# Optimization experiments

Hardware: AMD Instinct MI355X
Metric: run time of the kernel (lower is better)

The kernel has to match this reference:

```python
import jax, jax.numpy as jnp
import numpy as np

D_ATOM, D_PAIR, D_HID = 128, 64, 32
NF, NLOC = 1, 384


def setup_inputs() -> dict:
    key = jax.random.key(0)
    k1, k2, k3, k4, k5 = jax.random.split(key, 5)
    m = jax.random.normal(k1, (NF, NLOC, D_ATOM), dtype=jnp.float32)
    nlist = jax.random.randint(k2, (NF, NLOC, 32), 0, NLOC)
    op_mask = jnp.ones((1,), dtype=jnp.float32)
    op_norm = jnp.ones((1,), dtype=jnp.float32)
    # linear_in: d_atom -> 2*d_hid ; linear_out: d_hid**2 -> d_pair
    W_in = jax.random.normal(k3, (2 * D_HID, D_ATOM), dtype=jnp.float32) * 0.05
    b_in = jnp.zeros((2 * D_HID,), dtype=jnp.float32)
    W_out = jax.random.normal(k4, (D_PAIR, D_HID * D_HID), dtype=jnp.float32) * 0.05
    b_out = jnp.zeros((D_PAIR,), dtype=jnp.float32)
    return {"m": m, "nlist": nlist, "op_mask": op_mask, "op_norm": op_norm,
            "W_in": W_in, "b_in": b_in, "W_out": W_out, "b_out": b_out}


def reference(m, nlist, op_mask, op_norm, W_in, b_in, W_out, b_out):
    # ab: [nf, nloc, 2*d_hid]
    ab = jnp.einsum('fnd,hd->fnh', m, W_in) + b_in
    ab = ab * op_mask
    a, b = jnp.split(ab, 2, axis=-1)  # each [nf, nloc, d_hid]
    nf, nloc, d = a.shape
    # outer product: [nf, nloc, nloc, d_hid*d_hid]
    outer = jnp.einsum('fix,fjy->fijxy', a, b).reshape(nf, nloc, nloc, d * d)
    z = jnp.einsum('fijk,pk->fijp', outer, W_out) + b_out  # [nf, nloc, nloc, d_pair]
    return z * op_norm
```

## Files before the change

kernel.cpp:

```cpp
#include <hip/hip_runtime.h>

#define NLOC 384


__global__ __launch_bounds__(256) void k_ab(const float* __restrict__ m,
                                            const float* __restrict__ W_in,
                                            const float* __restrict__ b_in,
                                            const float* __restrict__ op_mask,
                                            float* __restrict__ ab) {
    const int t  = threadIdx.x;
    const int h  = t & 63;
    const int ng = __builtin_amdgcn_readfirstlane(t >> 6);
    const int n  = blockIdx.x * 4 + ng;
    const float* mrow = m + n * 128;
    const float* wrow = W_in + h * 128;
    float acc = 0.f;
#pragma unroll
    for (int dq = 0; dq < 32; ++dq) {
        const float4 w  = *reinterpret_cast<const float4*>(wrow + dq * 4);
        const float4 mv = *reinterpret_cast<const float4*>(mrow + dq * 4);
        acc += w.x * mv.x + w.y * mv.y + w.z * mv.z + w.w * mv.w;
    }
    ab[n * 64 + h] = (acc + b_in[h]) * op_mask[0];
}

__global__ __launch_bounds__(256) void k_T(const float* __restrict__ ab,
                                           const float* __restrict__ W_out,
                                           float* __restrict__ T) {
    const int t    = threadIdx.x;
    const int j    = blockIdx.x >> 1;
    const int half = blockIdx.x & 1;
    const int xp0  = half * 1024 + t * 4;
    const int x    = xp0 >> 6;
    const int p0   = xp0 & 63;

    const float* brow = ab + j * 64 + 32;
    float4 acc;
    float* accp = reinterpret_cast<float*>(&acc);
#pragma unroll 2
    for (int pp = 0; pp < 4; ++pp) {
        const float* wb = W_out + (p0 + pp) * 1024 + x * 32;
        float s = 0.f;
#pragma unroll
        for (int yq = 0; yq < 8; ++yq) {
            const float4 w = *reinterpret_cast<const float4*>(wb + yq * 4);
            s += brow[yq * 4 + 0] * w.x + brow[yq * 4 + 1] * w.y +
                 brow[yq * 4 + 2] * w.z + brow[yq * 4 + 3] * w.w;
        }
        accp[pp] = s;
    }
    *reinterpret_cast<float4*>(T + j * 2048 + xp0) = acc;
}

__global__ __launch_bounds__(256) void k_main3(const float* __restrict__ ab,
                                               const float* __restrict__ T,
                                               const float* __restrict__ b_out,
                                               const float* __restrict__ op_norm,
                                               float* __restrict__ out) {
    const int t    = threadIdx.x;
    const int lane = t & 63;
    const int wv   = __builtin_amdgcn_readfirstlane(t >> 6);
    const int jt   = blockIdx.x % 24;
    const int it   = blockIdx.x / 24;
    const int jq   = lane >> 4;
    const int p4   = (lane & 15) * 4;
    const int j    = jt * 16 + wv * 4 + jq;
    const int i0   = it * 16;

    __shared__ float a_sh[16][32];
    if (t < 128) {
        const int ii = t >> 3, xq8 = t & 7;
        *reinterpret_cast<float4*>(&a_sh[ii][xq8 * 4]) =
            *reinterpret_cast<const float4*>(ab + (i0 + ii) * 64 + xq8 * 4);
    }
    __syncthreads();

    const float4 bo  = *reinterpret_cast<const float4*>(b_out + p4);
    const float norm = op_norm[0];

    float4 acc[16];
#pragma unroll
    for (int i = 0; i < 16; ++i) acc[i] = bo;

    const float* Tj = T + j * 2048 + p4;

#pragma unroll 2
    for (int xq = 0; xq < 8; ++xq) {
        float4 t4[4];
#pragma unroll
        for (int s = 0; s < 4; ++s)
            t4[s] = *reinterpret_cast<const float4*>(Tj + (xq * 4 + s) * 64);
#pragma unroll
        for (int i = 0; i < 16; ++i) {
            const float4 av = *reinterpret_cast<const float4*>(&a_sh[i][xq * 4]);
            acc[i].x += av.x * t4[0].x + av.y * t4[1].x + av.z * t4[2].x + av.w * t4[3].x;
            acc[i].y += av.x * t4[0].y + av.y * t4[1].y + av.z * t4[2].y + av.w * t4[3].y;
            acc[i].z += av.x * t4[0].z + av.y * t4[1].z + av.z * t4[2].z + av.w * t4[3].z;
            acc[i].w += av.x * t4[0].w + av.y * t4[1].w + av.z * t4[2].w + av.w * t4[3].w;
        }
    }

#pragma unroll
    for (int i = 0; i < 16; ++i) {
        float4 r;
        r.x = acc[i].x * norm; r.y = acc[i].y * norm;
        r.z = acc[i].z * norm; r.w = acc[i].w * norm;
        *reinterpret_cast<float4*>(out + ((i0 + i) * NLOC + j) * 64 + p4) = r;
    }
}

extern "C" void kernel_launch(void* const* d_in, const int* in_sizes, int n_in,
                              void* d_out, int out_size, void* d_ws, size_t ws_size,
                              hipStream_t stream) {
    const float* m       = (const float*)d_in[0];
    const float* op_mask = (const float*)d_in[2];
    const float* op_norm = (const float*)d_in[3];
    const float* W_in    = (const float*)d_in[4];
    const float* b_in    = (const float*)d_in[5];
    const float* W_out   = (const float*)d_in[6];
    const float* b_out   = (const float*)d_in[7];
    float* out = (float*)d_out;

    float* ab = (float*)d_ws;
    float* T  = (float*)((char*)d_ws + 98304);

    k_ab   <<<96,  256, 0, stream>>>(m, W_in, b_in, op_mask, ab);
    k_T    <<<768, 256, 0, stream>>>(ab, W_out, T);
    k_main3<<<576, 256, 0, stream>>>(ab, T, b_out, op_norm, out);
}
```

Baseline: 109.9 us.

## Stage W_out tiles in LDS and reuse them across six j rows in k_T

k_T now loads a 16-row slice of W_out into shared memory once per block. Each thread keeps 32 weights in registers and computes outputs for six j values, so W_out is re-read far less often from global memory and the grid shrinks from 768 to 256 blocks. Each block now uses about 64KB of LDS, which lowers k_T occupancy, and the T stores become scalar and strided. k_main3 also gets a launch-bounds occupancy hint of 3 blocks per CU, which may constrain register allocation.

```diff
diff --git a/kernel.cpp b/kernel.cpp
--- a/kernel.cpp
+++ b/kernel.cpp
@@ -27,36 +27,50 @@
 __global__ __launch_bounds__(256) void k_T(const float* __restrict__ ab,
                                            const float* __restrict__ W_out,
                                            float* __restrict__ T) {
-    const int t    = threadIdx.x;
-    const int j    = blockIdx.x >> 1;
-    const int half = blockIdx.x & 1;
-    const int xp0  = half * 1024 + t * 4;
-    const int x    = xp0 >> 6;
-    const int p0   = xp0 & 63;
+    const int t  = threadIdx.x;
+    const int pt = blockIdx.x & 3;
+    const int jt = blockIdx.x >> 2;
+    __shared__ float Wsh[16][1028];
 
-    const float* brow = ab + j * 64 + 32;
-    float4 acc;
-    float* accp = reinterpret_cast<float*>(&acc);
-#pragma unroll 2
-    for (int pp = 0; pp < 4; ++pp) {
-        const float* wb = W_out + (p0 + pp) * 1024 + x * 32;
-        float s = 0.f;
 #pragma unroll
-        for (int yq = 0; yq < 8; ++yq) {
-            const float4 w = *reinterpret_cast<const float4*>(wb + yq * 4);
-            s += brow[yq * 4 + 0] * w.x + brow[yq * 4 + 1] * w.y +
-                 brow[yq * 4 + 2] * w.z + brow[yq * 4 + 3] * w.w;
+    for (int row = 0; row < 16; ++row) {
+        const float4 v = *reinterpret_cast<const float4*>(
+            W_out + (pt * 16 + row) * 1024 + t * 4);
+        *reinterpret_cast<float4*>(&Wsh[row][t * 4]) = v;
+    }
+    __syncthreads();
+
+    const int pl = t & 15;
+    const int xg = t >> 4;
+    const int p  = pt * 16 + pl;
+
+#pragma unroll
+    for (int xs = 0; xs < 2; ++xs) {
+        const int x = xg * 2 + xs;
+        float4 w[8];
+#pragma unroll
+        for (int yq = 0; yq < 8; ++yq)
+            w[yq] = *reinterpret_cast<const float4*>(&Wsh[pl][x * 32 + yq * 4]);
+#pragma unroll
+        for (int jl = 0; jl < 6; ++jl) {
+            const int j = jt * 6 + jl;
+            const float* brow = ab + j * 64 + 32;
+            float s = 0.f;
+#pragma unroll
+            for (int yq = 0; yq < 8; ++yq) {
+                s += brow[yq * 4 + 0] * w[yq].x + brow[yq * 4 + 1] * w[yq].y +
+                     brow[yq * 4 + 2] * w[yq].z + brow[yq * 4 + 3] * w[yq].w;
+            }
+            T[j * 2048 + x * 64 + p] = s;
         }
-        accp[pp] = s;
     }
-    *reinterpret_cast<float4*>(T + j * 2048 + xp0) = acc;
 }
 
-__global__ __launch_bounds__(256) void k_main3(const float* __restrict__ ab,
-                                               const float* __restrict__ T,
-                                               const float* __restrict__ b_out,
-                                               const float* __restrict__ op_norm,
-                                               float* __restrict__ out) {
+__global__ __launch_bounds__(256, 3) void k_main3(const float* __restrict__ ab,
+                                                  const float* __restrict__ T,
+                                                  const float* __restrict__ b_out,
+                                                  const float* __restrict__ op_norm,
+                                                  float* __restrict__ out) {
     const int t    = threadIdx.x;
     const int lane = t & 63;
     const int wv   = __builtin_amdgcn_readfirstlane(t >> 6);
@@ -125,6 +139,6 @@
     float* T  = (float*)((char*)d_ws + 98304);
 
     k_ab   <<<96,  256, 0, stream>>>(m, W_in, b_in, op_mask, ab);
-    k_T    <<<768, 256, 0, stream>>>(ab, W_out, T);
+    k_T    <<<256, 256, 0, stream>>>(ab, W_out, T);
     k_main3<<<576, 256, 0, stream>>>(ab, T, b_out, op_norm, out);
 }
```

Result: slower. 120.3 us (+9.4%).

## Reuse W_out registers across 12 j rows in T kernel; read a directly from global

Applied to the files above, without the earlier changes.

The T kernel now loads each thread's slice of W_out into registers once and reuses it for 12 consecutive j rows, so the grid drops from 768 blocks to 64. This removes the repeated W_out reloads. The main kernel drops its shared-memory staging of a and the barrier, and instead reads a values directly from global memory (wave-uniform scalar loads) one x at a time. The cost is fewer blocks and much higher register pressure in the T kernel (128 floats of weights per thread), and more, less-vectorised loads of a in the main kernel.

```diff
diff --git a/kernel.cpp b/kernel.cpp
--- a/kernel.cpp
+++ b/kernel.cpp
@@ -24,35 +24,45 @@
     ab[n * 64 + h] = (acc + b_in[h]) * op_mask[0];
 }
 
-__global__ __launch_bounds__(256) void k_T(const float* __restrict__ ab,
-                                           const float* __restrict__ W_out,
-                                           float* __restrict__ T) {
+__global__ __launch_bounds__(256) void k_T2(const float* __restrict__ ab,
+                                            const float* __restrict__ W_out,
+                                            float* __restrict__ T) {
     const int t    = threadIdx.x;
-    const int j    = blockIdx.x >> 1;
     const int half = blockIdx.x & 1;
+    const int jt   = blockIdx.x >> 1;
     const int xp0  = half * 1024 + t * 4;
     const int x    = xp0 >> 6;
     const int p0   = xp0 & 63;
 
-    const float* brow = ab + j * 64 + 32;
-    float4 acc;
-    float* accp = reinterpret_cast<float*>(&acc);
-#pragma unroll 2
-    for (int pp = 0; pp < 4; ++pp) {
-        const float* wb = W_out + (p0 + pp) * 1024 + x * 32;
-        float s = 0.f;
+    float4 w[4][8];
 #pragma unroll
-        for (int yq = 0; yq < 8; ++yq) {
-            const float4 w = *reinterpret_cast<const float4*>(wb + yq * 4);
-            s += brow[yq * 4 + 0] * w.x + brow[yq * 4 + 1] * w.y +
-                 brow[yq * 4 + 2] * w.z + brow[yq * 4 + 3] * w.w;
+    for (int c = 0; c < 4; ++c)
+#pragma unroll
+        for (int yq = 0; yq < 8; ++yq)
+            w[c][yq] = *reinterpret_cast<const float4*>(
+                W_out + (p0 + c) * 1024 + x * 32 + yq * 4);
+
+#pragma unroll
+    for (int jl = 0; jl < 12; ++jl) {
+        const int j = jt * 12 + jl;
+        const float* brow = ab + j * 64 + 32;
+        float4 acc = {0.f, 0.f, 0.f, 0.f};
+        float* accp = reinterpret_cast<float*>(&acc);
+#pragma unroll
+        for (int c = 0; c < 4; ++c) {
+            float s = 0.f;
+#pragma unroll
+            for (int yq = 0; yq < 8; ++yq) {
+                s += brow[yq * 4 + 0] * w[c][yq].x + brow[yq * 4 + 1] * w[c][yq].y +
+                     brow[yq * 4 + 2] * w[c][yq].z + brow[yq * 4 + 3] * w[c][yq].w;
+            }
+            accp[c] = s;
         }
-        accp[pp] = s;
+        *reinterpret_cast<float4*>(T + j * 2048 + xp0) = acc;
     }
-    *reinterpret_cast<float4*>(T + j * 2048 + xp0) = acc;
 }
 
-__global__ __launch_bounds__(256) void k_main3(const float* __restrict__ ab,
+__global__ __launch_bounds__(256) void k_main2(const float* __restrict__ ab,
                                                const float* __restrict__ T,
                                                const float* __restrict__ b_out,
                                                const float* __restrict__ op_norm,
@@ -67,14 +77,6 @@
     const int j    = jt * 16 + wv * 4 + jq;
     const int i0   = it * 16;
 
-    __shared__ float a_sh[16][32];
-    if (t < 128) {
-        const int ii = t >> 3, xq8 = t & 7;
-        *reinterpret_cast<float4*>(&a_sh[ii][xq8 * 4]) =
-            *reinterpret_cast<const float4*>(ab + (i0 + ii) * 64 + xq8 * 4);
-    }
-    __syncthreads();
-
     const float4 bo  = *reinterpret_cast<const float4*>(b_out + p4);
     const float norm = op_norm[0];
 
@@ -82,21 +84,19 @@
 #pragma unroll
     for (int i = 0; i < 16; ++i) acc[i] = bo;
 
-    const float* Tj = T + j * 2048 + p4;
+    const float* Tj   = T + j * 2048 + p4;
+    const float* arow = ab + i0 * 64;
 
-#pragma unroll 2
-    for (int xq = 0; xq < 8; ++xq) {
-        float4 t4[4];
-#pragma unroll
-        for (int s = 0; s < 4; ++s)
-            t4[s] = *reinterpret_cast<const float4*>(Tj + (xq * 4 + s) * 64);
+#pragma unroll 4
+    for (int x = 0; x < 32; ++x) {
+        const float4 t4 = *reinterpret_cast<const float4*>(Tj + x * 64);
 #pragma unroll
         for (int i = 0; i < 16; ++i) {
-            const float4 av = *reinterpret_cast<const float4*>(&a_sh[i][xq * 4]);
-            acc[i].x += av.x * t4[0].x + av.y * t4[1].x + av.z * t4[2].x + av.w * t4[3].x;
-            acc[i].y += av.x * t4[0].y + av.y * t4[1].y + av.z * t4[2].y + av.w * t4[3].y;
-            acc[i].z += av.x * t4[0].z + av.y * t4[1].z + av.z * t4[2].z + av.w * t4[3].z;
-            acc[i].w += av.x * t4[0].w + av.y * t4[1].w + av.z * t4[2].w + av.w * t4[3].w;
+            const float a = arow[i * 64 + x];
+            acc[i].x += a * t4.x;
+            acc[i].y += a * t4.y;
+            acc[i].z += a * t4.z;
+            acc[i].w += a * t4.w;
         }
     }
 
@@ -125,6 +125,6 @@
     float* T  = (float*)((char*)d_ws + 98304);
 
     k_ab   <<<96,  256, 0, stream>>>(m, W_in, b_in, op_mask, ab);
-    k_T    <<<768, 256, 0, stream>>>(ab, W_out, T);
-    k_main3<<<576, 256, 0, stream>>>(ab, T, b_out, op_norm, out);
+    k_T2   <<<64,  256, 0, stream>>>(ab, W_out, T);
+    k_main2<<<576, 256, 0, stream>>>(ab, T, b_out, op_norm, out);
 }
```

After: 107.3 us. 2.4% less time.
